# Performance work log

Measured on AMD Instinct MI355X. Metric: run time of the kernel, lower is better.

## Reference

```python
import jax, jax.numpy as jnp
import numpy as np

B, S, T = 64, 512, 256  # batch, seq_len, num_tags


def setup_inputs() -> dict:
    key = jax.random.key(0)
    k1, k2, k3, k4 = jax.random.split(key, 4)
    emissions = jax.random.normal(k1, (B, S, T), dtype=jnp.float32)
    tags = jax.random.randint(k2, (B, S), 0, T, dtype=jnp.int32)
    mask = jnp.ones((B, S), dtype=bool)
    # nn.init.uniform_(-0.01, 0.01) as in reset_parameters()
    transitions = jax.random.uniform(k3, (T, T), minval=-0.01, maxval=0.01, dtype=jnp.float32)
    tse = jax.random.uniform(k4, (T + 2, T + 2), minval=-0.01, maxval=0.01, dtype=jnp.float32)
    tse = tse.at[T + 1, T].set(-10000.0)  # transitions[end_tag, start_tag] = -10000
    return {"emissions": emissions, "tags": tags, "mask": mask,
            "transitions": transitions, "transitions_with_start_end": tse}


def reference(emissions, tags, mask, transitions, transitions_with_start_end):
    Bv, Sv, Tv = emissions.shape
    start, end = Tv, Tv + 1

    # ---- forward algorithm (log partition), faithful to the torch recurrence:
    # new[b, j] = alpha[b, j] + logsumexp_k( trans[k, j] + emit_t[b, k] )
    # (the mask line fv*mask + fv*~mask in the original is a no-op)
    alpha0 = emissions[:, 0] + transitions_with_start_end[start, :Tv]

    def step(alpha, em_t):  # em_t: [B, T]
        lse = jax.nn.logsumexp(transitions[None, :, :] + em_t[:, :, None], axis=1)  # [B, T]
        return alpha + lse, None

    ems = jnp.swapaxes(emissions[:, 1:], 0, 1)  # [S-1, B, T]
    alpha, _ = jax.lax.scan(step, alpha0, ems)
    forward_score = jax.nn.logsumexp(alpha + transitions_with_start_end[:Tv, end], axis=1)  # [B]

    # ---- gold path score
    mf = mask.astype(emissions.dtype)
    emit = jnp.take_along_axis(emissions, tags[:, :, None].astype(jnp.int32), axis=2)[:, :, 0]  # [B, S]
    score = transitions_with_start_end[start, tags[:, 0]]
    score = score + jnp.sum(emit * mf, axis=1)
    score = score + jnp.sum(transitions[tags[:, 1:], tags[:, :-1]] * mf[:, 1:], axis=1)
    last_idx = jnp.sum(mask.astype(jnp.int32), axis=1) - 1  # [B]
    last_tags = jnp.take_along_axis(tags, last_idx[:, None], axis=1)[:, 0]
    score = score + transitions_with_start_end[last_tags, end]

    return forward_score - score  # negative log-likelihood per batch element, [B]
```

## Files before the change

### kernel.cpp

```cpp
#include <hip/hip_runtime.h>
#include <cstdint>

#define B_ 64
#define S_ 512
#define T_ 256
#define TP2 258

#define BM 64
#define BK 32
#define LDA 40
#define LDB 40
#define GEMMB ((B_ * S_) / BM)

typedef __attribute__((ext_vector_type(8))) short short8;
typedef __attribute__((ext_vector_type(4))) float f32x4;

__device__ __forceinline__ ushort f2bf(float f) {
    union { float f; uint32_t u; } c; c.f = f;
    uint32_t u = c.u;
    u += 0x7FFFu + ((u >> 16) & 1u);
    return (ushort)(u >> 16);
}

__global__ void prep_w(const float* __restrict__ trans, ushort* __restrict__ wt,
                       float* __restrict__ accb, int* __restrict__ tickets) {
    int k = blockIdx.x;
    int n = threadIdx.x;
    wt[n * T_ + k] = f2bf(__expf(trans[k * T_ + n]));
    if (k < B_) accb[k * T_ + n] = 0.f;
    else if (k == B_ && n < B_) tickets[n] = 0;
}

__global__ __launch_bounds__(256, 3) void gemm_lse(
    const float* __restrict__ em, const int* __restrict__ tags,
    const float* __restrict__ trans, const float* __restrict__ tse,
    const ushort* __restrict__ wt, float* __restrict__ accb,
    int* __restrict__ tickets, float* __restrict__ gold,
    float* __restrict__ out)
{
    __shared__ ushort Alds[BM * LDA];
    __shared__ ushort Blds[T_ * LDB];
    __shared__ float red[8];
    __shared__ int winflag;

    int blk = blockIdx.x;
    int tid = threadIdx.x;
    int batch;

    if (blk >= GEMMB) {
        batch = blk - GEMMB;
        const int* tg = tags + batch * S_;
        float sc = 0.f;
        for (int s = tid; s < S_; s += 256) {
            int t = tg[s];
            sc += em[((long)batch * S_ + s) * T_ + t];
            if (s >= 1) sc += trans[t * T_ + tg[s - 1]];
        }
        if (tid == 0) {
            sc += tse[T_ * TP2 + tg[0]];
            sc += tse[tg[S_ - 1] * TP2 + (T_ + 1)];
        }
        #pragma unroll
        for (int o = 32; o; o >>= 1) sc += __shfl_xor(sc, o);
        if ((tid & 63) == 0) red[tid >> 6] = sc;
        __syncthreads();
        if (tid == 0) gold[batch] = red[0] + red[1] + red[2] + red[3];
    } else {
        long r0   = (long)blk * BM;
        batch     = blk >> 3;
        bool has_s0 = (blk & 7) == 0;

        int wave = tid >> 6;
        int lane = tid & 63;
        int quad = lane >> 4;
        int l15  = lane & 15;

        f32x4 acc[4][4];
        #pragma unroll
        for (int i = 0; i < 4; ++i)
            #pragma unroll
            for (int j = 0; j < 4; ++j)
                acc[i][j] = (f32x4){0.f, 0.f, 0.f, 0.f};

        int srow = tid >> 2;
        int skc  = (tid & 3) * 8;

        for (int kt = 0; kt < T_ / BK; ++kt) {
            int k0 = kt * BK;
            {
                const float* src = em + (r0 + srow) * T_ + k0 + skc;
                float4 va = *(const float4*)(src);
                float4 vb = *(const float4*)(src + 4);
                union { ushort u[8]; uint4 v; } pk;
                pk.u[0] = f2bf(__expf(va.x)); pk.u[1] = f2bf(__expf(va.y));
                pk.u[2] = f2bf(__expf(va.z)); pk.u[3] = f2bf(__expf(va.w));
                pk.u[4] = f2bf(__expf(vb.x)); pk.u[5] = f2bf(__expf(vb.y));
                pk.u[6] = f2bf(__expf(vb.z)); pk.u[7] = f2bf(__expf(vb.w));
                *(uint4*)&Alds[srow * LDA + skc] = pk.v;
            }
            #pragma unroll
            for (int p = 0; p < 4; ++p) {
                int idx = tid + p * 256;
                uint4 v = *(const uint4*)&wt[(idx >> 2) * T_ + k0 + (idx & 3) * 8];
                *(uint4*)&Blds[(idx >> 2) * LDB + (idx & 3) * 8] = v;
            }
            __syncthreads();

            short8 af[4], bf[4];
            #pragma unroll
            for (int i = 0; i < 4; ++i)
                af[i] = *(const short8*)&Alds[(i * 16 + l15) * LDA + quad * 8];
            #pragma unroll
            for (int j = 0; j < 4; ++j)
                bf[j] = *(const short8*)&Blds[(wave * 64 + j * 16 + l15) * LDB + quad * 8];
            #pragma unroll
            for (int i = 0; i < 4; ++i)
                #pragma unroll
                for (int j = 0; j < 4; ++j)
                    acc[i][j] = __builtin_amdgcn_mfma_f32_16x16x32_bf16(af[i], bf[j], acc[i][j], 0, 0, 0);
            __syncthreads();
        }

        #pragma unroll
        for (int j = 0; j < 4; ++j) {
            float s = 0.f;
            #pragma unroll
            for (int i = 0; i < 4; ++i) {
                f32x4 a = acc[i][j];
                #pragma unroll
                for (int v = 0; v < 4; ++v) {
                    bool skip = has_s0 && (i == 0) && (quad == 0) && (v == 0);
                    if (!skip) s += __logf(a[v]);
                }
            }
            s += __shfl_xor(s, 16);
            s += __shfl_xor(s, 32);
            if (lane < 16)
                atomicAdd(&accb[batch * T_ + wave * 64 + j * 16 + lane], s);
        }
    }

    __syncthreads();
    if (tid == 0) {
        int t = __hip_atomic_fetch_add(&tickets[batch], 1,
                                       __ATOMIC_ACQ_REL, __HIP_MEMORY_SCOPE_AGENT);
        winflag = (t == 8);
    }
    __syncthreads();
    if (winflag) {
        int b = batch;
        int j = tid;
        int w = j >> 6;
        float aj = __hip_atomic_load(&accb[b * T_ + j],
                                     __ATOMIC_ACQUIRE, __HIP_MEMORY_SCOPE_AGENT);
        float v = em[(long)b * S_ * T_ + j] + tse[T_ * TP2 + j]
                + aj + tse[j * TP2 + (T_ + 1)];

        float m = v;
        #pragma unroll
        for (int o = 32; o; o >>= 1) m = fmaxf(m, __shfl_xor(m, o));
        if ((j & 63) == 0) red[w] = m;
        __syncthreads();
        m = fmaxf(fmaxf(red[0], red[1]), fmaxf(red[2], red[3]));

        float e = __expf(v - m);
        #pragma unroll
        for (int o = 32; o; o >>= 1) e += __shfl_xor(e, o);
        if ((j & 63) == 0) red[4 + w] = e;
        __syncthreads();
        if (j == 0) {
            float fwd = m + __logf(red[4] + red[5] + red[6] + red[7]);
            float g = __hip_atomic_load(&gold[b],
                                        __ATOMIC_ACQUIRE, __HIP_MEMORY_SCOPE_AGENT);
            out[b] = fwd - g;
        }
    }
}

extern "C" void kernel_launch(void* const* d_in, const int* in_sizes, int n_in,
                              void* d_out, int out_size, void* d_ws, size_t ws_size,
                              hipStream_t stream) {
    const float* em    = (const float*)d_in[0];
    const int*   tags  = (const int*)d_in[1];
    const float* trans = (const float*)d_in[3];
    const float* tse   = (const float*)d_in[4];
    float* out = (float*)d_out;

    ushort* wt      = (ushort*)d_ws;
    float*  accb    = (float*)((char*)d_ws + 131072);
    int*    tickets = (int*)((char*)d_ws + 196608);
    float*  gold    = (float*)((char*)d_ws + 196864);

    prep_w<<<T_, T_, 0, stream>>>(trans, wt, accb, tickets);
    gemm_lse<<<GEMMB + B_, 256, 0, stream>>>(em, tags, trans, tse,
                                             wt, accb, tickets, gold, out);
}
```

Before: 102.7 us.

## Stage full A tile in LDS once and read B fragments directly from global

Each block now loads and exponentiates its whole 64x256 emission tile into LDS up front with batched loads, which removes the per-k-step barrier pairs. The B operand (exp of transitions, bf16) is no longer staged through LDS; each wave reads its MFMA fragments straight from global/L2. This is meant to cut synchronisation and LDS traffic and to expose more memory-level parallelism. In exchange it uses more LDS per block and issues uncoalesced 16-byte global reads for B that depend on cache hits.

```diff
diff --git a/kernel.cpp b/kernel.cpp
--- a/kernel.cpp
+++ b/kernel.cpp
@@ -7,9 +7,7 @@
 #define TP2 258
 
 #define BM 64
-#define BK 32
-#define LDA 40
-#define LDB 40
+#define LDAT 272
 #define GEMMB ((B_ * S_) / BM)
 
 typedef __attribute__((ext_vector_type(8))) short short8;
@@ -38,8 +36,7 @@
     int* __restrict__ tickets, float* __restrict__ gold,
     float* __restrict__ out)
 {
-    __shared__ ushort Alds[BM * LDA];
-    __shared__ ushort Blds[T_ * LDB];
+    __shared__ ushort Alds[BM * LDAT];
     __shared__ float red[8];
     __shared__ int winflag;
 
@@ -75,6 +72,31 @@
         int quad = lane >> 4;
         int l15  = lane & 15;
 
+        int srow = tid >> 2;
+        int skc  = (tid & 3) * 8;
+        const float* src = em + (r0 + srow) * T_ + skc;
+
+        #pragma unroll
+        for (int h = 0; h < 2; ++h) {
+            float4 v[8];
+            #pragma unroll
+            for (int g = 0; g < 4; ++g) {
+                v[2 * g]     = *(const float4*)(src + (h * 4 + g) * 32);
+                v[2 * g + 1] = *(const float4*)(src + (h * 4 + g) * 32 + 4);
+            }
+            #pragma unroll
+            for (int g = 0; g < 4; ++g) {
+                float4 a = v[2 * g], b = v[2 * g + 1];
+                union { ushort u[8]; uint4 vv; } pk;
+                pk.u[0] = f2bf(__expf(a.x)); pk.u[1] = f2bf(__expf(a.y));
+                pk.u[2] = f2bf(__expf(a.z)); pk.u[3] = f2bf(__expf(a.w));
+                pk.u[4] = f2bf(__expf(b.x)); pk.u[5] = f2bf(__expf(b.y));
+                pk.u[6] = f2bf(__expf(b.z)); pk.u[7] = f2bf(__expf(b.w));
+                *(uint4*)&Alds[srow * LDAT + (h * 4 + g) * 32 + skc] = pk.vv;
+            }
+        }
+        __syncthreads();
+
         f32x4 acc[4][4];
         #pragma unroll
         for (int i = 0; i < 4; ++i)
@@ -82,43 +104,23 @@
             for (int j = 0; j < 4; ++j)
                 acc[i][j] = (f32x4){0.f, 0.f, 0.f, 0.f};
 
-        int srow = tid >> 2;
-        int skc  = (tid & 3) * 8;
+        const ushort* bsrc = wt + (wave * 64 + l15) * T_ + quad * 8;
 
-        for (int kt = 0; kt < T_ / BK; ++kt) {
-            int k0 = kt * BK;
-            {
-                const float* src = em + (r0 + srow) * T_ + k0 + skc;
-                float4 va = *(const float4*)(src);
-                float4 vb = *(const float4*)(src + 4);
-                union { ushort u[8]; uint4 v; } pk;
-                pk.u[0] = f2bf(__expf(va.x)); pk.u[1] = f2bf(__expf(va.y));
-                pk.u[2] = f2bf(__expf(va.z)); pk.u[3] = f2bf(__expf(va.w));
-                pk.u[4] = f2bf(__expf(vb.x)); pk.u[5] = f2bf(__expf(vb.y));
-                pk.u[6] = f2bf(__expf(vb.z)); pk.u[7] = f2bf(__expf(vb.w));
-                *(uint4*)&Alds[srow * LDA + skc] = pk.v;
-            }
-            #pragma unroll
-            for (int p = 0; p < 4; ++p) {
-                int idx = tid + p * 256;
-                uint4 v = *(const uint4*)&wt[(idx >> 2) * T_ + k0 + (idx & 3) * 8];
-                *(uint4*)&Blds[(idx >> 2) * LDB + (idx & 3) * 8] = v;
-            }
-            __syncthreads();
-
+        #pragma unroll 2
+        for (int kt = 0; kt < 8; ++kt) {
+            int k0 = kt * 32;
             short8 af[4], bf[4];
             #pragma unroll
+            for (int j = 0; j < 4; ++j)
+                bf[j] = *(const short8*)(bsrc + j * 16 * T_ + k0);
+            #pragma unroll
             for (int i = 0; i < 4; ++i)
-                af[i] = *(const short8*)&Alds[(i * 16 + l15) * LDA + quad * 8];
-            #pragma unroll
-            for (int j = 0; j < 4; ++j)
-                bf[j] = *(const short8*)&Blds[(wave * 64 + j * 16 + l15) * LDB + quad * 8];
+                af[i] = *(const short8*)&Alds[(i * 16 + l15) * LDAT + k0 + quad * 8];
             #pragma unroll
             for (int i = 0; i < 4; ++i)
                 #pragma unroll
                 for (int j = 0; j < 4; ++j)
                     acc[i][j] = __builtin_amdgcn_mfma_f32_16x16x32_bf16(af[i], bf[j], acc[i][j], 0, 0, 0);
-            __syncthreads();
         }
 
         #pragma unroll
```

Result: no change. 103.6 us (+0.9%).
